# Kernel tuning notes

Hardware: AMD Instinct MI355X
Metric: run time of the kernel (lower is better)

Reference implementation:

```python
import jax, jax.numpy as jnp
import numpy as np

NEIGH = 16  # default neigh in __init__


def setup_inputs() -> dict:
    key = jax.random.key(0)
    kx, kuv = jax.random.split(key)
    B, M = 8, 4096
    X = jax.random.normal(kx, (B, M, 3), dtype=jnp.float32)
    uv = jax.random.uniform(kuv, (B, M, 2), dtype=jnp.float32)
    return {"X": X, "uv": uv}


def reference(X, uv):
    # Pairwise squared distances in parameter (uv) space: (B, M, M)
    dm = jnp.sum((uv[:, :, None, :] - uv[:, None, :, :]) ** 2, axis=-1)
    # k nearest neighbours (smallest distances) -> indices (B, M, K)
    _, k_inds = jax.lax.top_k(-dm, NEIGH)
    # Gather 3D neighbourhoods: (B, M, K, 3)
    knns = jax.vmap(lambda x, idx: x[idx])(X, k_inds)
    # Covariance per point: center then K x 3 outer products -> (B, M, 3, 3)
    centered = knns - jnp.mean(knns, axis=2, keepdims=True)
    cov = jnp.einsum('bmki,bmkj->bmij', centered, centered)
    # Symmetric 3x3 eigenvalues; torch sorts descending, eigvalsh is ascending
    eig = jnp.linalg.eigvalsh(cov)
    fff = eig[..., ::-1]  # (B, M, 3), descending
    return fff
```

## Files before the change

### kernel.cpp

```cpp
#include <hip/hip_runtime.h>
#include <hip/hip_bf16.h>
#include <math.h>

typedef unsigned long long u64;
typedef unsigned int u32;
typedef unsigned short u16;

constexpr int NB  = 8;
constexpr int NM  = 4096;
constexpr int KNN = 16;
constexpr int WPB = 8;
constexpr int QPB = WPB * 2;
constexpr int BLK = WPB * 64;
constexpr int GC  = 16;
constexpr int NC  = GC * GC;
constexpr int CSST = NC + 1;
constexpr int SLG = 8;

constexpr size_t WS_UVS = 0;
constexpr size_t WS_IDX = 262144;
constexpr size_t WS_CS  = 327680;

__device__ __forceinline__ u64 shflx64(u64 v, int m) {
  unsigned lo = (unsigned)v, hi = (unsigned)(v >> 32);
  lo = __shfl_xor(lo, m, 64);
  hi = __shfl_xor(hi, m, 64);
  return ((u64)hi << 32) | lo;
}

__device__ __forceinline__ int rfl(int x) {
  return __builtin_amdgcn_readfirstlane(x);
}

__device__ __forceinline__ int lanes_below(u64 m) {
  return (int)__builtin_amdgcn_mbcnt_hi((u32)(m >> 32),
             __builtin_amdgcn_mbcnt_lo((u32)m, 0u));
}

__device__ __forceinline__ u32 gmask(u64 m, int lane) {
  return (lane & 32) ? (u32)(m >> 32) : (u32)m;
}

__global__ __launch_bounds__(1024)
void bin_pts(const float* __restrict__ uv, float2* __restrict__ uvS,
             u16* __restrict__ idxS, u32* __restrict__ cs) {
  __shared__ u32 cnt[NC];
  __shared__ u32 offs[NC];
  __shared__ u32 wtot[4];
  const int bb  = blockIdx.x;
  const int tid = threadIdx.x;

  if (tid < NC) cnt[tid] = 0;
  __syncthreads();

  float2 c4[4];
  int cell[4];
  #pragma unroll
  for (int i = 0; i < 4; ++i) {
    const int p = tid + i * 1024;
    const float2 c = ((const float2*)(uv + (size_t)bb * NM * 2))[p];
    int cx = (int)(c.x * (float)GC); cx = cx > GC - 1 ? GC - 1 : (cx < 0 ? 0 : cx);
    int cy = (int)(c.y * (float)GC); cy = cy > GC - 1 ? GC - 1 : (cy < 0 ? 0 : cy);
    c4[i] = c; cell[i] = cy * GC + cx;
    atomicAdd(&cnt[cell[i]], 1u);
  }
  __syncthreads();

  if (tid < NC) {
    const int lane = tid & 63;
    u32 inc = cnt[tid];
    #pragma unroll
    for (int o = 1; o < 64; o <<= 1) {
      const u32 t = __shfl_up(inc, o, 64);
      if (lane >= o) inc += t;
    }
    offs[tid] = inc;
    if (lane == 63) wtot[tid >> 6] = inc;
  }
  __syncthreads();
  if (tid < NC) {
    const int w = tid >> 6;
    u32 base = 0;
    #pragma unroll
    for (int i = 0; i < 3; ++i) base += (i < w) ? wtot[i] : 0;
    const u32 excl = base + offs[tid] - cnt[tid];
    cs[bb * CSST + tid] = excl;
    offs[tid] = excl;
    if (tid == 0) cs[bb * CSST + NC] = NM;
  }
  __syncthreads();

  #pragma unroll
  for (int i = 0; i < 4; ++i) {
    const int p = tid + i * 1024;
    const u32 pos = atomicAdd(&offs[cell[i]], 1u);
    uvS[(size_t)bb * NM + pos]  = c4[i];
    idxS[(size_t)bb * NM + pos] = (u16)p;
  }
}

__global__ __launch_bounds__(BLK, 8)
void knn_eig(const float* __restrict__ X, const float* __restrict__ uv,
             const float2* __restrict__ uvS, const u16* __restrict__ idxS,
             const u32* __restrict__ cs, float* __restrict__ out) {
  __shared__ u64 surv[WPB][64];

  const int tid  = threadIdx.x;
  const int lane = tid & 63;
  const int sub  = lane & 31;
  const int half = lane >> 5;
  const int wv   = tid >> 6;
  const int bb   = blockIdx.x >> 8;
  const int q    = ((blockIdx.x & 255) << 4) + (wv << 1) + half;

  const float qu = uv[((size_t)bb * NM + q) * 2];
  const float qv = uv[((size_t)bb * NM + q) * 2 + 1];
  int cxv = (int)(qu * (float)GC); cxv = cxv > GC - 1 ? GC - 1 : (cxv < 0 ? 0 : cxv);
  int cyv = (int)(qv * (float)GC); cyv = cyv > GC - 1 ? GC - 1 : (cyv < 0 ? 0 : cyv);
  const u32* csb = cs + bb * CSST;
  const float2* uvb = uvS + (size_t)bb * NM;
  const u16* idxb = idxS + (size_t)bb * NM;

  float d[SLG];
  int   ca[SLG];
  #pragma unroll
  for (int t = 0; t < SLG; ++t) d[t] = 1e30f;

  constexpr float TAU1 = 0.0017f;
  constexpr float TAU2 = 0.00390625f;

  int total, tsw;
  int cnt = 0;
  {
    const int x0 = cxv > 0 ? cxv - 1 : 0, x1 = cxv < GC - 1 ? cxv + 1 : GC - 1;
    const int y0 = cyv > 0 ? cyv - 1 : 0, y1 = cyv < GC - 1 ? cyv + 1 : GC - 1;
    const int rs0 = (int)csb[y0 * GC + x0];
    const int rc0 = (int)csb[y0 * GC + x1 + 1] - rs0;
    const int rs1 = (int)csb[(y0 + 1) * GC + x0];
    const int rc1 = rc0 + (int)csb[(y0 + 1) * GC + x1 + 1] - rs1;
    const bool ok2 = (y0 + 2) <= y1;
    const int rs2 = (int)csb[ok2 ? ((y0 + 2) * GC + x0) : 0];
    const int re2 = (int)csb[ok2 ? ((y0 + 2) * GC + x1 + 1) : 0];
    total = rc1 + (ok2 ? (re2 - rs2) : 0);
    int ts = (total + 31) >> 5;
    tsw = rfl(max(ts, __shfl_xor(ts, 32, 64)));
    #pragma unroll
    for (int t = 0; t < SLG; ++t) {
      if (t >= tsw) break;
      const int L = t * 32 + sub;
      int addr = rs0 + L;
      if (L >= rc0) addr = rs1 + (L - rc0);
      if (L >= rc1) addr = rs2 + (L - rc1);
      float dd = 1e30f;
      if (L < total) {
        const float2 c = uvb[addr];
        const float dx = __fsub_rn(qu, c.x);
        const float dy = __fsub_rn(qv, c.y);
        dd = __fadd_rn(__fmul_rn(dx, dx), __fmul_rn(dy, dy));
      }
      d[t] = dd; ca[t] = addr;
      cnt += (int)__popc(gmask(__ballot(dd <= TAU1), lane));
    }
  }

  float hi2 = (cnt < KNN) ? TAU2 : TAU1;
  if (__any(cnt < KNN)) {
    int c2 = 0;
    #pragma unroll
    for (int t = 0; t < SLG; ++t) {
      if (t >= tsw) break;
      c2 += (int)__popc(gmask(__ballot(d[t] <= TAU2), lane));
    }
    if (cnt < KNN) cnt = c2;
  }

  {
    float lo = 0.f;
    for (int it = 0; __any(cnt > 32) && it < 40; ++it) {
      const float mid = 0.5f * (lo + hi2);
      int c = 0;
      #pragma unroll
      for (int t = 0; t < SLG; ++t) {
        if (t >= tsw) break;
        c += (int)__popc(gmask(__ballot(cnt > 32 && d[t] <= mid), lane));
      }
      if (cnt > 32) {
        if (!(mid > lo && mid < hi2)) { cnt = 32; }
        else if (c >= KNN) { hi2 = mid; cnt = c; }
        else lo = mid;
      }
    }
  }

  u64* sb = surv[wv];
  {
    int base = 0;
    #pragma unroll
    for (int t = 0; t < SLG; ++t) {
      if (t >= tsw) break;
      const bool p = d[t] <= hi2;
      const u32 mg = gmask(__ballot(p), lane);
      if (p) {
        const int pos = base + (int)__popc(mg & ((1u << sub) - 1u));
        if (pos < 32)
          sb[(half << 5) + pos] = ((u64)__float_as_uint(d[t]) << 32) | (u64)idxb[ca[t]];
      }
      base += (int)__popc(mg);
    }
  }

  if (__any(cnt < KNN)) {
    for (int g = 0; g < 2; ++g) {
      const int need = rfl((__shfl(cnt, g * 32, 64) < KNN) ? 1 : 0);
      if (!need) continue;
      const float gu = __shfl(qu, g * 32, 64);
      const float gv = __shfl(qv, g * 32, 64);
      const int gcx = rfl(__shfl(cxv, g * 32, 64));
      const int gcy = rfl(__shfl(cyv, g * 32, 64));
      float ghi = 0.f;
      int gcnt = 0, gts = 0, gtotal = 0;
      for (int h = 2; h <= 5; ++h) {
        const int x0 = gcx - h < 0 ? 0 : gcx - h, x1 = gcx + h > GC - 1 ? GC - 1 : gcx + h;
        const int y0 = gcy - h < 0 ? 0 : gcy - h, y1 = gcy + h > GC - 1 ? GC - 1 : gcy + h;
        int rstart[7], rcum[7];
        int cum = 0;
        #pragma unroll
        for (int r = 0; r < 7; ++r) {
          const int y = y0 + r;
          const bool ok = (y <= y1);
          const u32 s = csb[ok ? (y * GC + x0) : 0];
          const u32 e = csb[ok ? (y * GC + x1 + 1) : 0];
          rstart[r] = (int)s;
          cum += ok ? (int)(e - s) : 0;
          rcum[r] = cum;
        }
        gtotal = cum;
        gts = (gtotal + 63) >> 6; if (gts > SLG) gts = SLG;
        const float hv = (float)h * 0.0625f;
        ghi = hv * hv;
        gcnt = 0;
        for (int t = 0; t < gts; ++t) {
          const int L = t * 64 + lane;
          int addr = rstart[0] + L;
          #pragma unroll
          for (int r = 1; r < 7; ++r)
            if (L >= rcum[r - 1]) addr = rstart[r] + (L - rcum[r - 1]);
          float dd = 1e30f;
          if (L < gtotal) {
            const float2 c = uvb[addr];
            const float dx = __fsub_rn(gu, c.x);
            const float dy = __fsub_rn(gv, c.y);
            dd = __fadd_rn(__fmul_rn(dx, dx), __fmul_rn(dy, dy));
          }
          d[t] = dd; ca[t] = addr;
          gcnt += (int)__popcll(__ballot(dd <= ghi));
        }
        if (rfl(gcnt) >= KNN) break;
      }
      {
        float lo = 0.f;
        for (int it = 0; rfl(gcnt) > 32 && it < 40; ++it) {
          const float mid = 0.5f * (lo + ghi);
          if (!(mid > lo && mid < ghi)) break;
          int c = 0;
          for (int t = 0; t < gts; ++t) c += (int)__popcll(__ballot(d[t] <= mid));
          if (c >= KNN) { ghi = mid; gcnt = c; } else lo = mid;
        }
      }
      int base = 0;
      for (int t = 0; t < gts; ++t) {
        const bool p = d[t] <= ghi;
        const u64 m = __ballot(p);
        if (p) {
          const int pos = base + lanes_below(m);
          if (pos < 32)
            sb[(g << 5) + pos] = ((u64)__float_as_uint(d[t]) << 32) | (u64)idxb[ca[t]];
        }
        base += (int)__popcll(m);
      }
      if (half == g) cnt = gcnt < 32 ? gcnt : 32;
    }
  }

  const int S = cnt < 32 ? cnt : 32;
  u64 v = (sub < S) ? sb[lane] : ~0ull;
  if (cnt > KNN) {
    const int dir4 = (lane >> 4) & 1;
    #pragma unroll
    for (int k = 2; k <= 16; k <<= 1) {
      #pragma unroll
      for (int j = k >> 1; j > 0; j >>= 1) {
        const u64 o = shflx64(v, j);
        const bool up = (((lane & k & 15) == 0) != (dir4 != 0));
        const bool km = (((lane & j) == 0) == up);
        v = ((v < o) == km) ? v : o;
      }
    }
    const u64 o = shflx64(v, 16);
    const bool km = ((lane & 16) == 0);
    v = ((v < o) == km) ? v : o;
  }

  float x = 0.f, y = 0.f, z = 0.f;
  if ((lane & 16) == 0) {
    const int idx = (int)(u32)v & 0xFFF;
    const float* Xp = X + ((size_t)bb * NM + idx) * 3;
    x = Xp[0]; y = Xp[1]; z = Xp[2];
  }
  float sx = x, sy = y, sz = z;
  float sxx = x * x, sxy = x * y, sxz = x * z;
  float syy = y * y, syz = y * z, szz = z * z;
  #pragma unroll
  for (int o = 8; o > 0; o >>= 1) {
    sx  += __shfl_xor(sx,  o, 64);  sy  += __shfl_xor(sy,  o, 64);
    sz  += __shfl_xor(sz,  o, 64);  sxx += __shfl_xor(sxx, o, 64);
    sxy += __shfl_xor(sxy, o, 64);  sxz += __shfl_xor(sxz, o, 64);
    syy += __shfl_xor(syy, o, 64);  syz += __shfl_xor(syz, o, 64);
    szz += __shfl_xor(szz, o, 64);
  }

  const float mx = sx * 0.0625f, my = sy * 0.0625f, mz = sz * 0.0625f;
  const float c00 = sxx - 16.f * mx * mx;
  const float c11 = syy - 16.f * my * my;
  const float c22 = szz - 16.f * mz * mz;
  const float c01 = sxy - 16.f * mx * my;
  const float c02 = sxz - 16.f * mx * mz;
  const float c12 = syz - 16.f * my * mz;

  const float tr = c00 + c11 + c22;
  const float q3 = tr * (1.f / 3.f);
  const float b0 = c00 - q3, b1 = c11 - q3, b2 = c22 - q3;
  const float p2 = b0 * b0 + b1 * b1 + b2 * b2 +
                   2.f * (c01 * c01 + c02 * c02 + c12 * c12);
  float e0, e1, e2;
  if (p2 < 1e-30f) {
    e0 = e1 = e2 = q3;
  } else {
    const float p  = sqrtf(p2 * (1.f / 6.f));
    const float ip = 1.f / p;
    const float m00 = b0 * ip, m11 = b1 * ip, m22 = b2 * ip;
    const float m01 = c01 * ip, m02 = c02 * ip, m12 = c12 * ip;
    const float det = m00 * (m11 * m22 - m12 * m12)
                    - m01 * (m01 * m22 - m12 * m02)
                    + m02 * (m01 * m12 - m11 * m02);
    float r = 0.5f * det;
    r = fminf(1.f, fmaxf(-1.f, r));
    const float phi = acosf(r) * (1.f / 3.f);
    float sphi, cphi;
    __sincosf(phi, &sphi, &cphi);
    e0 = q3 + 2.f * p * cphi;
    e2 = q3 + 2.f * p * (-0.5f * cphi - 0.8660254037844386f * sphi);
    e1 = tr - e0 - e2;
  }

  if (sub == 0) {
    float* op = out + ((size_t)bb * NM + q) * 3;
    op[0] = e0; op[1] = e1; op[2] = e2;
  }
}

extern "C" void kernel_launch(void* const* d_in, const int* in_sizes, int n_in,
                              void* d_out, int out_size, void* d_ws, size_t ws_size,
                              hipStream_t stream) {
  const float* X  = (const float*)d_in[0];
  const float* uv = (const float*)d_in[1];
  float* out = (float*)d_out;
  char* ws = (char*)d_ws;
  float2* uvS = (float2*)(ws + WS_UVS);
  u16*    idxS = (u16*)(ws + WS_IDX);
  u32*    csP  = (u32*)(ws + WS_CS);

  bin_pts<<<dim3(NB), dim3(1024), 0, stream>>>(uv, uvS, idxS, csP);
  knn_eig<<<dim3(NB * NM / QPB), dim3(BLK), 0, stream>>>(X, uv, uvS, idxS, csP, out);
}
```

Before: 30.11 us.

## Process four queries per wavefront with 16-lane groups and two-register bitonic sort

```diff
diff --git a/kernel.cpp b/kernel.cpp
--- a/kernel.cpp
+++ b/kernel.cpp
@@ -10,12 +10,14 @@
 constexpr int NM  = 4096;
 constexpr int KNN = 16;
 constexpr int WPB = 8;
-constexpr int QPB = WPB * 2;
+constexpr int QPW = 4;
+constexpr int QPB = WPB * QPW;
 constexpr int BLK = WPB * 64;
 constexpr int GC  = 16;
 constexpr int NC  = GC * GC;
 constexpr int CSST = NC + 1;
-constexpr int SLG = 8;
+constexpr int SLG = 12;
+constexpr int SLC = 8;
 
 constexpr size_t WS_UVS = 0;
 constexpr size_t WS_IDX = 262144;
@@ -27,18 +29,13 @@
   hi = __shfl_xor(hi, m, 64);
   return ((u64)hi << 32) | lo;
 }
-
-__device__ __forceinline__ int rfl(int x) {
-  return __builtin_amdgcn_readfirstlane(x);
-}
-
+__device__ __forceinline__ int rfl(int x) { return __builtin_amdgcn_readfirstlane(x); }
 __device__ __forceinline__ int lanes_below(u64 m) {
   return (int)__builtin_amdgcn_mbcnt_hi((u32)(m >> 32),
              __builtin_amdgcn_mbcnt_lo((u32)m, 0u));
 }
-
-__device__ __forceinline__ u32 gmask(u64 m, int lane) {
-  return (lane & 32) ? (u32)(m >> 32) : (u32)m;
+__device__ __forceinline__ u32 gm16(u64 m, int lane) {
+  return (u32)(m >> ((lane >> 4) << 4)) & 0xFFFFu;
 }
 
 __global__ __launch_bounds__(1024)
@@ -103,15 +100,15 @@
 void knn_eig(const float* __restrict__ X, const float* __restrict__ uv,
              const float2* __restrict__ uvS, const u16* __restrict__ idxS,
              const u32* __restrict__ cs, float* __restrict__ out) {
-  __shared__ u64 surv[WPB][64];
+  __shared__ u64 surv[WPB][QPW * 32];
 
   const int tid  = threadIdx.x;
   const int lane = tid & 63;
-  const int sub  = lane & 31;
-  const int half = lane >> 5;
+  const int sub  = lane & 15;
+  const int g4   = lane >> 4;
   const int wv   = tid >> 6;
-  const int bb   = blockIdx.x >> 8;
-  const int q    = ((blockIdx.x & 255) << 4) + (wv << 1) + half;
+  const int bb   = blockIdx.x >> 7;
+  const int q    = ((blockIdx.x & 127) << 5) + (wv << 2) + g4;
 
   const float qu = uv[((size_t)bb * NM + q) * 2];
   const float qv = uv[((size_t)bb * NM + q) * 2 + 1];
@@ -122,32 +119,35 @@
   const u16* idxb = idxS + (size_t)bb * NM;
 
   float d[SLG];
-  int   ca[SLG];
   #pragma unroll
   for (int t = 0; t < SLG; ++t) d[t] = 1e30f;
 
   constexpr float TAU1 = 0.0017f;
   constexpr float TAU2 = 0.00390625f;
 
-  int total, tsw;
+  int rs0, rc0, rs1, rc1, rs2, total, tsw;
+  bool ovf;
   int cnt = 0;
   {
     const int x0 = cxv > 0 ? cxv - 1 : 0, x1 = cxv < GC - 1 ? cxv + 1 : GC - 1;
     const int y0 = cyv > 0 ? cyv - 1 : 0, y1 = cyv < GC - 1 ? cyv + 1 : GC - 1;
-    const int rs0 = (int)csb[y0 * GC + x0];
-    const int rc0 = (int)csb[y0 * GC + x1 + 1] - rs0;
-    const int rs1 = (int)csb[(y0 + 1) * GC + x0];
-    const int rc1 = rc0 + (int)csb[(y0 + 1) * GC + x1 + 1] - rs1;
+    rs0 = (int)csb[y0 * GC + x0];
+    rc0 = (int)csb[y0 * GC + x1 + 1] - rs0;
+    rs1 = (int)csb[(y0 + 1) * GC + x0];
+    rc1 = rc0 + (int)csb[(y0 + 1) * GC + x1 + 1] - rs1;
     const bool ok2 = (y0 + 2) <= y1;
-    const int rs2 = (int)csb[ok2 ? ((y0 + 2) * GC + x0) : 0];
+    rs2 = (int)csb[ok2 ? ((y0 + 2) * GC + x0) : 0];
     const int re2 = (int)csb[ok2 ? ((y0 + 2) * GC + x1 + 1) : 0];
     total = rc1 + (ok2 ? (re2 - rs2) : 0);
-    int ts = (total + 31) >> 5;
-    tsw = rfl(max(ts, __shfl_xor(ts, 32, 64)));
+    ovf = total > SLG * 16;
+    int ts = (total + 15) >> 4; if (ts > SLG) ts = SLG;
+    int m1 = max(ts, __shfl_xor(ts, 16, 64));
+    m1 = max(m1, __shfl_xor(m1, 32, 64));
+    tsw = rfl(m1);
     #pragma unroll
     for (int t = 0; t < SLG; ++t) {
       if (t >= tsw) break;
-      const int L = t * 32 + sub;
+      const int L = t * 16 + sub;
       int addr = rs0 + L;
       if (L >= rc0) addr = rs1 + (L - rc0);
       if (L >= rc1) addr = rs2 + (L - rc1);
@@ -158,9 +158,10 @@
         const float dy = __fsub_rn(qv, c.y);
         dd = __fadd_rn(__fmul_rn(dx, dx), __fmul_rn(dy, dy));
       }
-      d[t] = dd; ca[t] = addr;
-      cnt += (int)__popc(gmask(__ballot(dd <= TAU1), lane));
-    }
+      d[t] = dd;
+      cnt += (int)__popc(gm16(__ballot(dd <= TAU1), lane));
+    }
+    if (ovf) cnt = 0;
   }
 
   float hi2 = (cnt < KNN) ? TAU2 : TAU1;
@@ -169,20 +170,20 @@
     #pragma unroll
     for (int t = 0; t < SLG; ++t) {
       if (t >= tsw) break;
-      c2 += (int)__popc(gmask(__ballot(d[t] <= TAU2), lane));
-    }
-    if (cnt < KNN) cnt = c2;
+      c2 += (int)__popc(gm16(__ballot(d[t] <= TAU2), lane));
+    }
+    if (cnt < KNN && !ovf) cnt = c2;
   }
 
   {
-    float lo = 0.f;
+    float lo = (hi2 > TAU1) ? TAU1 : 0.f;
     for (int it = 0; __any(cnt > 32) && it < 40; ++it) {
       const float mid = 0.5f * (lo + hi2);
       int c = 0;
       #pragma unroll
       for (int t = 0; t < SLG; ++t) {
         if (t >= tsw) break;
-        c += (int)__popc(gmask(__ballot(cnt > 32 && d[t] <= mid), lane));
+        c += (int)__popc(gm16(__ballot(cnt > 32 && d[t] <= mid), lane));
       }
       if (cnt > 32) {
         if (!(mid > lo && mid < hi2)) { cnt = 32; }
@@ -199,24 +200,31 @@
     for (int t = 0; t < SLG; ++t) {
       if (t >= tsw) break;
       const bool p = d[t] <= hi2;
-      const u32 mg = gmask(__ballot(p), lane);
+      const u32 mg = gm16(__ballot(p), lane);
       if (p) {
         const int pos = base + (int)__popc(mg & ((1u << sub) - 1u));
-        if (pos < 32)
-          sb[(half << 5) + pos] = ((u64)__float_as_uint(d[t]) << 32) | (u64)idxb[ca[t]];
+        if (pos < 32) {
+          const int L = t * 16 + sub;
+          int addr = rs0 + L;
+          if (L >= rc0) addr = rs1 + (L - rc0);
+          if (L >= rc1) addr = rs2 + (L - rc1);
+          sb[(g4 << 5) + pos] = ((u64)__float_as_uint(d[t]) << 32) | (u64)idxb[addr];
+        }
       }
       base += (int)__popc(mg);
     }
   }
 
   if (__any(cnt < KNN)) {
-    for (int g = 0; g < 2; ++g) {
-      const int need = rfl((__shfl(cnt, g * 32, 64) < KNN) ? 1 : 0);
-      if (!need) continue;
-      const float gu = __shfl(qu, g * 32, 64);
-      const float gv = __shfl(qv, g * 32, 64);
-      const int gcx = rfl(__shfl(cxv, g * 32, 64));
-      const int gcy = rfl(__shfl(cyv, g * 32, 64));
+    #pragma unroll 1
+    for (int g = 0; g < QPW; ++g) {
+      if (!rfl((__shfl(cnt, g << 4, 64) < KNN) ? 1 : 0)) continue;
+      const float gu = __shfl(qu, g << 4, 64);
+      const float gv = __shfl(qv, g << 4, 64);
+      const int gcx = rfl(__shfl(cxv, g << 4, 64));
+      const int gcy = rfl(__shfl(cyv, g << 4, 64));
+      float gd[SLC];
+      int   ga[SLC];
       float ghi = 0.f;
       int gcnt = 0, gts = 0, gtotal = 0;
       for (int h = 2; h <= 5; ++h) {
@@ -235,11 +243,14 @@
           rcum[r] = cum;
         }
         gtotal = cum;
-        gts = (gtotal + 63) >> 6; if (gts > SLG) gts = SLG;
+        int t0 = (gtotal + 63) >> 6; if (t0 > SLC) t0 = SLC;
+        gts = rfl(t0);
         const float hv = (float)h * 0.0625f;
         ghi = hv * hv;
         gcnt = 0;
-        for (int t = 0; t < gts; ++t) {
+        #pragma unroll
+        for (int t = 0; t < SLC; ++t) {
+          if (t >= gts) break;
           const int L = t * 64 + lane;
           int addr = rstart[0] + L;
           #pragma unroll
@@ -252,7 +263,7 @@
             const float dy = __fsub_rn(gv, c.y);
             dd = __fadd_rn(__fmul_rn(dx, dx), __fmul_rn(dy, dy));
           }
-          d[t] = dd; ca[t] = addr;
+          gd[t] = dd; ga[t] = addr;
           gcnt += (int)__popcll(__ballot(dd <= ghi));
         }
         if (rfl(gcnt) >= KNN) break;
@@ -263,50 +274,54 @@
           const float mid = 0.5f * (lo + ghi);
           if (!(mid > lo && mid < ghi)) break;
           int c = 0;
-          for (int t = 0; t < gts; ++t) c += (int)__popcll(__ballot(d[t] <= mid));
+          #pragma unroll
+          for (int t = 0; t < SLC; ++t) {
+            if (t >= gts) break;
+            c += (int)__popcll(__ballot(gd[t] <= mid));
+          }
           if (c >= KNN) { ghi = mid; gcnt = c; } else lo = mid;
         }
       }
       int base = 0;
-      for (int t = 0; t < gts; ++t) {
-        const bool p = d[t] <= ghi;
+      #pragma unroll
+      for (int t = 0; t < SLC; ++t) {
+        if (t >= gts) break;
+        const bool p = gd[t] <= ghi;
         const u64 m = __ballot(p);
         if (p) {
           const int pos = base + lanes_below(m);
           if (pos < 32)
-            sb[(g << 5) + pos] = ((u64)__float_as_uint(d[t]) << 32) | (u64)idxb[ca[t]];
+            sb[(g << 5) + pos] = ((u64)__float_as_uint(gd[t]) << 32) | (u64)idxb[ga[t]];
         }
         base += (int)__popcll(m);
       }
-      if (half == g) cnt = gcnt < 32 ? gcnt : 32;
+      if (g4 == g) cnt = gcnt < 32 ? gcnt : 32;
     }
   }
 
   const int S = cnt < 32 ? cnt : 32;
-  u64 v = (sub < S) ? sb[lane] : ~0ull;
-  if (cnt > KNN) {
-    const int dir4 = (lane >> 4) & 1;
-    #pragma unroll
-    for (int k = 2; k <= 16; k <<= 1) {
-      #pragma unroll
-      for (int j = k >> 1; j > 0; j >>= 1) {
-        const u64 o = shflx64(v, j);
-        const bool up = (((lane & k & 15) == 0) != (dir4 != 0));
-        const bool km = (((lane & j) == 0) == up);
-        v = ((v < o) == km) ? v : o;
-      }
-    }
-    const u64 o = shflx64(v, 16);
-    const bool km = ((lane & 16) == 0);
-    v = ((v < o) == km) ? v : o;
-  }
-
-  float x = 0.f, y = 0.f, z = 0.f;
-  if ((lane & 16) == 0) {
-    const int idx = (int)(u32)v & 0xFFF;
-    const float* Xp = X + ((size_t)bb * NM + idx) * 3;
-    x = Xp[0]; y = Xp[1]; z = Xp[2];
-  }
+  const int sbase = g4 << 5;
+  u64 v0 = (sub < S) ? sb[sbase + sub] : ~0ull;
+  u64 v1 = (16 + sub < S) ? sb[sbase + 16 + sub] : ~0ull;
+  #pragma unroll
+  for (int k = 2; k <= 16; k <<= 1) {
+    #pragma unroll
+    for (int j = k >> 1; j > 0; j >>= 1) {
+      const u64 o0 = shflx64(v0, j);
+      const u64 o1 = shflx64(v1, j);
+      const bool up = ((sub & k) == 0);
+      const bool j0 = ((sub & j) == 0);
+      const bool km0 = (j0 == up);
+      const bool km1 = (j0 != up);
+      v0 = ((v0 < o0) == km0) ? v0 : o0;
+      v1 = ((v1 < o1) == km1) ? v1 : o1;
+    }
+  }
+  const u64 v = (v0 < v1) ? v0 : v1;
+
+  const int idx = (int)(u32)v & 0xFFF;
+  const float* Xp = X + ((size_t)bb * NM + idx) * 3;
+  const float x = Xp[0], y = Xp[1], z = Xp[2];
   float sx = x, sy = y, sz = z;
   float sxx = x * x, sxy = x * y, sxz = x * z;
   float syy = y * y, syz = y * z, szz = z * z;
```

Measured after the change: 27.51 us. -8.6%, faster.
